# Performance work log

Measured on AMD Instinct MI355X. Metric: run time of the kernel, lower is better.

The kernel has to match this reference:

```python
import jax, jax.numpy as jnp
import numpy as np

DIM = 2048
NUM_HEADS = 16
HEAD_DIM = DIM // NUM_HEADS  # 128
B, L = 2, 2048


def setup_inputs() -> dict:
    key = jax.random.key(0)
    ks = jax.random.split(key, 5)
    x = jax.random.normal(ks[0], (B, L, DIM), dtype=jnp.float32)
    # genuine RoPE tables: inv_freq over half the head dim
    half = HEAD_DIM // 2
    inv_freq = 1.0 / (10000.0 ** (jnp.arange(half, dtype=jnp.float32) / half))
    ang = jnp.arange(L, dtype=jnp.float32)[:, None] * inv_freq[None, :]  # (L, half)
    cos = jnp.cos(ang)[:, None, :]  # (L, 1, half) broadcasts over (B,L,H,half)
    sin = jnp.sin(ang)[:, None, :]
    def dw_init(k, shape):
        fan_in, fan_out = shape
        std = 1.0 / np.sqrt(fan_in) * min(1.0, np.sqrt(fan_out / fan_in))
        return jax.random.normal(k, shape, dtype=jnp.float32) * std
    Wq = dw_init(ks[1], (DIM, DIM))
    Wk = dw_init(ks[2], (DIM, HEAD_DIM))
    Wv = dw_init(ks[3], (DIM, HEAD_DIM))
    Wo = dw_init(ks[4], (DIM, DIM))  # random instead of zeros so output is nontrivial
    return {"x": x, "cos": cos, "sin": sin, "Wq": Wq, "Wk": Wk, "Wv": Wv, "Wo": Wo}


def apply_rotary_emb(x, cos, sin):
    x1, x2 = jnp.split(x, 2, axis=-1)
    return jnp.concatenate([x1 * cos + x2 * sin, x1 * -sin + x2 * cos], axis=-1)


def rms_norm(x):
    return x * jax.lax.rsqrt(jnp.mean(x * x, axis=-1, keepdims=True) + 1e-6)


def reference(x, cos, sin, Wq, Wk, Wv, Wo):
    Bb, Ll, _ = x.shape
    q = (x @ Wq).reshape(Bb, Ll, NUM_HEADS, HEAD_DIM)  # (B,L,H,D)
    k = (x @ Wk)  # (B,L,D)  single KV head (MQA)
    v = (x @ Wv)  # (B,L,D)
    q = rms_norm(apply_rotary_emb(q, cos, sin))
    k = rms_norm(apply_rotary_emb(k[:, :, None, :], cos, sin))[:, :, 0, :]  # (B,L,D)
    scale = 1.0 / jnp.sqrt(jnp.asarray(HEAD_DIM, dtype=x.dtype))
    # scores without materializing broadcasted K: (B,H,Lq,Lk)
    scores = jnp.einsum('bqhd,bkd->bhqk', q, k) * scale
    causal = jnp.tril(jnp.ones((Ll, Ll), dtype=jnp.bool_))
    scores = jnp.where(causal[None, None], scores, jnp.asarray(-jnp.inf, dtype=scores.dtype))
    attn = jax.nn.softmax(scores, axis=-1)
    out = jnp.einsum('bhqk,bkd->bqhd', attn, v).reshape(Bb, Ll, DIM)
    return out @ Wo
```

## Files before the change

### kernel.cpp

```cpp
#include <hip/hip_runtime.h>

#define DIM 2048
#define NH 16
#define HD 128
#define BB 2
#define LL 2048
#define MROWS (BB * LL)
#define NKV 2304
#define NT 32

typedef __attribute__((ext_vector_type(8))) short short8;
typedef __attribute__((ext_vector_type(4))) float floatx4;

__device__ inline ushort f2bf(float f) {
    union { float f; unsigned u; } v; v.f = f;
    unsigned r = v.u + 0x7FFFu + ((v.u >> 16) & 1u);
    return (ushort)(r >> 16);
}

__device__ __forceinline__ ushort f2bf_fast(float f) {
    __bf16 h = (__bf16)f;
    return __builtin_bit_cast(unsigned short, h);
}

#define GL16(g, l)                                                         \
    __builtin_amdgcn_global_load_lds(                                      \
        (const __attribute__((address_space(1))) unsigned int*)(g),        \
        (__attribute__((address_space(3))) unsigned int*)(l), 16, 0, 0)

__device__ __forceinline__ short8 ld8(const ushort* p) {
    return *reinterpret_cast<const short8*>(p);
}

__global__ __launch_bounds__(256) void prep(const float* __restrict__ x,
                                            ushort* __restrict__ xb,
                                            const float* __restrict__ Wq,
                                            const float* __restrict__ Wk,
                                            const float* __restrict__ Wv,
                                            const float* __restrict__ Wo,
                                            ushort* __restrict__ Wcatt,
                                            ushort* __restrict__ Wot) {
    __shared__ ushort T[64][72];
    const int bid = blockIdx.x;
    const int tid = threadIdx.x;
    if (bid < 4096) {
        size_t i = ((size_t)bid * 256 + tid) * 8;
        float4 a = *reinterpret_cast<const float4*>(x + i);
        float4 b = *reinterpret_cast<const float4*>(x + i + 4);
        ushort o[8] = {f2bf(a.x), f2bf(a.y), f2bf(a.z), f2bf(a.w),
                       f2bf(b.x), f2bf(b.y), f2bf(b.z), f2bf(b.w)};
        *reinterpret_cast<uint4*>(xb + i) = *reinterpret_cast<uint4*>(o);
        return;
    }
    const int wb = bid - 4096;
    const float* in;
    ushort* out;
    int in_ld, c0, r0;
    const int out_ld = 2048;
    if (wb < 1024) {
        in = Wq; out = Wcatt; in_ld = 2048;
        c0 = (wb & 31) * 64; r0 = (wb >> 5) * 64;
    } else if (wb < 2048) {
        int t = wb - 1024;
        in = Wo; out = Wot; in_ld = 2048;
        c0 = (t & 31) * 64; r0 = (t >> 5) * 64;
    } else if (wb < 2112) {
        int t = wb - 2048;
        in = Wk; out = Wcatt + (size_t)2048 * 2048; in_ld = 128;
        c0 = (t & 1) * 64; r0 = (t >> 1) * 64;
    } else {
        int t = wb - 2112;
        in = Wv; out = Wcatt + (size_t)2176 * 2048; in_ld = 128;
        c0 = (t & 1) * 64; r0 = (t >> 1) * 64;
    }
#pragma unroll
    for (int rep = 0; rep < 4; ++rep) {
        int idx = tid + rep * 256;
        int r = idx >> 4, c4 = idx & 15;
        float4 f = *reinterpret_cast<const float4*>(
            in + (size_t)(r0 + r) * in_ld + c0 + c4 * 4);
        T[r][c4 * 4 + 0] = f2bf(f.x);
        T[r][c4 * 4 + 1] = f2bf(f.y);
        T[r][c4 * 4 + 2] = f2bf(f.z);
        T[r][c4 * 4 + 3] = f2bf(f.w);
    }
    __syncthreads();
#pragma unroll
    for (int rep = 0; rep < 4; ++rep) {
        int idx = tid + rep * 256;
        int cr = idx >> 4, rc4 = idx & 15;
        uint a0 = (uint)T[rc4 * 4 + 0][cr] | ((uint)T[rc4 * 4 + 1][cr] << 16);
        uint a1 = (uint)T[rc4 * 4 + 2][cr] | ((uint)T[rc4 * 4 + 3][cr] << 16);
        uint2 val = {a0, a1};
        *reinterpret_cast<uint2*>(
            out + (size_t)(c0 + cr) * out_ld + r0 + rc4 * 4) = val;
    }
}

__global__ __launch_bounds__(512)
__attribute__((amdgpu_waves_per_eu(2, 2)))
void gemm2pq(const ushort* __restrict__ A,
             const ushort* __restrict__ Bt,
             float* __restrict__ Y, int N) {
    __shared__ __attribute__((aligned(16))) ushort lds[51200];
    const int tid = threadIdx.x;
    const int lane = tid & 63;
    const int w = tid >> 6;
    const int col = lane & 15, quad = lane >> 4;
    const int sel = col & 7;
    const int L = blockIdx.y * 16 + blockIdx.x;
    const int x8 = L & 7, jj = L >> 3;
    const int bx = (x8 & 1) * 8 + (jj & 7);
    const int by = (x8 >> 1) * 4 + (jj >> 3);
    const int m0 = by * 256, n0 = bx * 144;

    const int r0 = tid >> 3;
    const int gc0 = (tid & 7) ^ (r0 & 7);
    const uint offA = (uint)(m0 + r0) * 2048u + (uint)gc0 * 8u;
    const uint offB = (uint)(n0 + r0) * 2048u + (uint)gc0 * 8u;

    floatx4 acc[2][9];
#pragma unroll
    for (int mt = 0; mt < 2; ++mt)
#pragma unroll
        for (int nt = 0; nt < 9; ++nt) acc[mt][nt] = (floatx4){0.f, 0.f, 0.f, 0.f};

    const int aoff0 = w * 2048 + col * 64;
    const int boff0 = 16384 + col * 64;
    const int koff0 = (quad ^ sel) * 8;
    const int koff1 = ((4 + quad) ^ sel) * 8;

    auto stage = [&](ushort* lbase, int t) {
        if (t >= NT) return;
        uint tk = (uint)t * 64u;
#pragma unroll
        for (int rep = 0; rep < 4; ++rep)
            GL16(A + offA + rep * 131072u + tk,
                 lbase + (size_t)(tid + rep * 512) * 8);
#pragma unroll
        for (int rep = 0; rep < 2; ++rep)
            GL16(Bt + offB + rep * 131072u + tk,
                 lbase + 16384 + (size_t)(tid + rep * 512) * 8);
        if (tid < 128)
            GL16(Bt + offB + 262144u + tk,
                 lbase + 16384 + (size_t)(tid + 1024) * 8);
    };

    stage(lds, 0);
    asm volatile("s_waitcnt vmcnt(0)" ::: "memory");
    __builtin_amdgcn_s_barrier();

#pragma unroll 2
    for (int t = 0; t < NT; ++t) {
        ushort* lb = lds + (t & 1) * 25600;
        ushort* lbn = lds + ((t + 1) & 1) * 25600;

        short8 a0[2], b0[9];
#pragma unroll
        for (int mt = 0; mt < 2; ++mt)
            a0[mt] = ld8(lb + aoff0 + mt * 1024 + koff0);
#pragma unroll
        for (int nt = 0; nt < 9; ++nt)
            b0[nt] = ld8(lb + boff0 + nt * 1024 + koff0);
        stage(lbn, t + 1);
        __builtin_amdgcn_s_setprio(1);
#pragma unroll
        for (int mt = 0; mt < 2; ++mt)
#pragma unroll
            for (int nt = 0; nt < 9; ++nt)
                acc[mt][nt] = __builtin_amdgcn_mfma_f32_16x16x32_bf16(
                    a0[mt], b0[nt], acc[mt][nt], 0, 0, 0);
        __builtin_amdgcn_s_setprio(0);

        short8 a1[2], b1[9];
#pragma unroll
        for (int mt = 0; mt < 2; ++mt)
            a1[mt] = ld8(lb + aoff0 + mt * 1024 + koff1);
#pragma unroll
        for (int nt = 0; nt < 9; ++nt)
            b1[nt] = ld8(lb + boff0 + nt * 1024 + koff1);
        __builtin_amdgcn_s_setprio(1);
#pragma unroll
        for (int mt = 0; mt < 2; ++mt)
#pragma unroll
            for (int nt = 0; nt < 9; ++nt)
                acc[mt][nt] = __builtin_amdgcn_mfma_f32_16x16x32_bf16(
                    a1[mt], b1[nt], acc[mt][nt], 0, 0, 0);
        __builtin_amdgcn_s_setprio(0);
        asm volatile("s_waitcnt vmcnt(0)" ::: "memory");
        __builtin_amdgcn_s_barrier();
    }

#pragma unroll
    for (int mt = 0; mt < 2; ++mt)
#pragma unroll
        for (int nt = 0; nt < 9; ++nt)
#pragma unroll
            for (int rr = 0; rr < 4; ++rr)
                Y[(size_t)(m0 + w * 32 + mt * 16 + quad * 4 + rr) * N + n0 +
                  nt * 16 + col] = acc[mt][nt][rr];
}

template <int U>
__device__ __forceinline__ void stage_po(const ushort* __restrict__ A,
                                         const ushort* __restrict__ Bt,
                                         ushort* lbase, uint offA, uint offB,
                                         int t) {
    if (t >= NT) return;
    const ushort* g = (U < 2) ? Bt : A;
    uint off = ((U < 2) ? offB : offA) + ((U == 1) ? 128u * 2048u : 0u) +
               (uint)t * 64u;
    ushort* l = lbase + U * 8192;
    GL16(g + off, l + (size_t)threadIdx.x * 8);
    GL16(g + off + 64u * 2048u, l + (size_t)(threadIdx.x + 512) * 8);
}

__global__ __launch_bounds__(512)
__attribute__((amdgpu_waves_per_eu(2, 2)))
void gemm2pw(const ushort* __restrict__ A,
             const ushort* __restrict__ Bt,
             float* __restrict__ Y, int N) {
    __shared__ __attribute__((aligned(16))) ushort lds[49152];
    const int tid = threadIdx.x;
    const int lane = tid & 63;
    const int w = tid >> 6;
    const int wm = w >> 2, wn = w & 3;
    const int col = lane & 15, quad = lane >> 4;
    const int sel = col & 7;
    const int L = blockIdx.y * 8 + blockIdx.x;
    const int x8 = L & 7, jj = L >> 3;
    const int bx = (x8 & 1) * 4 + (jj & 3);
    const int by = (x8 >> 1) * 8 + (jj >> 2);
    const int m0 = by * 128, n0 = bx * 256;

    const int r0 = tid >> 3;
    const int gc0 = (tid & 7) ^ (r0 & 7);
    const uint offA = (uint)(m0 + r0) * 2048u + (uint)gc0 * 8u;
    const uint offB = (uint)(n0 + r0) * 2048u + (uint)gc0 * 8u;

    floatx4 acc[4][4];
#pragma unroll
    for (int mt = 0; mt < 4; ++mt)
#pragma unroll
        for (int nt = 0; nt < 4; ++nt) acc[mt][nt] = (floatx4){0.f, 0.f, 0.f, 0.f};

    const int aoff0 = 16384 + wm * 4096 + col * 64;
    const int boff0 = (wn >> 1) * 8192 + ((wn & 1) * 64 + col) * 64;
    const int koff0 = (quad ^ sel) * 8;
    const int koff1 = ((4 + quad) ^ sel) * 8;

    stage_po<0>(A, Bt, lds, offA, offB, 0);
    stage_po<1>(A, Bt, lds, offA, offB, 0);
    stage_po<2>(A, Bt, lds, offA, offB, 0);
    asm volatile("s_waitcnt vmcnt(0)" ::: "memory");
    __builtin_amdgcn_s_barrier();

#pragma unroll 2
    for (int t = 0; t < NT; ++t) {
        ushort* lb = lds + (t & 1) * 24576;
        ushort* lbn = lds + ((t + 1) & 1) * 24576;

        short8 a0[4], b0[4];
#pragma unroll
        for (int mt = 0; mt < 4; ++mt)
            a0[mt] = ld8(lb + aoff0 + mt * 1024 + koff0);
#pragma unroll
        for (int nt = 0; nt < 4; ++nt)
            b0[nt] = ld8(lb + boff0 + nt * 1024 + koff0);
        stage_po<0>(A, Bt, lbn, offA, offB, t + 1);
        stage_po<1>(A, Bt, lbn, offA, offB, t + 1);
        stage_po<2>(A, Bt, lbn, offA, offB, t + 1);
        __builtin_amdgcn_s_setprio(1);
#pragma unroll
        for (int mt = 0; mt < 4; ++mt)
#pragma unroll
            for (int nt = 0; nt < 4; ++nt)
                acc[mt][nt] = __builtin_amdgcn_mfma_f32_16x16x32_bf16(
                    a0[mt], b0[nt], acc[mt][nt], 0, 0, 0);
        __builtin_amdgcn_s_setprio(0);

        short8 a1[4], b1[4];
#pragma unroll
        for (int mt = 0; mt < 4; ++mt)
            a1[mt] = ld8(lb + aoff0 + mt * 1024 + koff1);
#pragma unroll
        for (int nt = 0; nt < 4; ++nt)
            b1[nt] = ld8(lb + boff0 + nt * 1024 + koff1);
        __builtin_amdgcn_s_setprio(1);
#pragma unroll
        for (int mt = 0; mt < 4; ++mt)
#pragma unroll
            for (int nt = 0; nt < 4; ++nt)
                acc[mt][nt] = __builtin_amdgcn_mfma_f32_16x16x32_bf16(
                    a1[mt], b1[nt], acc[mt][nt], 0, 0, 0);
        __builtin_amdgcn_s_setprio(0);
        asm volatile("s_waitcnt vmcnt(0)" ::: "memory");
        __builtin_amdgcn_s_barrier();
    }

#pragma unroll
    for (int mt = 0; mt < 4; ++mt)
#pragma unroll
        for (int nt = 0; nt < 4; ++nt)
#pragma unroll
            for (int rr = 0; rr < 4; ++rr)
                Y[(size_t)(m0 + wm * 64 + mt * 16 + quad * 4 + rr) * N + n0 +
                  wn * 64 + nt * 16 + col] = acc[mt][nt][rr];
}

__device__ __forceinline__ void rope_row(const float* __restrict__ in,
                                         ushort* __restrict__ outb,
                                         const float* __restrict__ cosb,
                                         const float* __restrict__ sinb,
                                         int row, int heads, int in_ld,
                                         int lane) {
    int token = row / heads, head = row % heads;
    int l = token & (LL - 1);
    const float* p = in + (size_t)token * in_ld + head * HD;
    float x1 = p[lane];
    float x2 = p[lane + 64];
    float c = cosb[l * 64 + lane];
    float s = sinb[l * 64 + lane];
    float o1 = x1 * c + x2 * s;
    float o2 = -x1 * s + x2 * c;
    float ss = o1 * o1 + o2 * o2;
#pragma unroll
    for (int off = 32; off > 0; off >>= 1) ss += __shfl_xor(ss, off);
    float r = rsqrtf(ss * (1.0f / 128.0f) + 1e-6f);
    outb[(size_t)row * HD + lane] = f2bf(o1 * r);
    outb[(size_t)row * HD + lane + 64] = f2bf(o2 * r);
}

__global__ __launch_bounds__(256) void rope_vt(const float* __restrict__ qkv,
                                               ushort* __restrict__ qb,
                                               ushort* __restrict__ kb,
                                               ushort* __restrict__ vt,
                                               const float* __restrict__ cosb,
                                               const float* __restrict__ sinb) {
    __shared__ ushort T[64][72];
    const int bid = blockIdx.x;
    const int tid = threadIdx.x;
    const int lane = tid & 63;
    if (bid < 16384) {
        int row = bid * 4 + (tid >> 6);
        rope_row(qkv, qb, cosb, sinb, row, NH, NKV, lane);
        return;
    }
    if (bid < 17408) {
        int row = (bid - 16384) * 4 + (tid >> 6);
        rope_row(qkv + DIM, kb, cosb, sinb, row, 1, MROWS == 0 ? 1 : 1, lane),
            rope_row(qkv + DIM, kb, cosb, sinb, row, 1, NKV, lane);
        return;
    }
    const int t = bid - 17408;
    const int l0 = (t & 31) * 64, d0 = ((t >> 5) & 1) * 64, b = t >> 6;
    const float* v = qkv + DIM + HD;
#pragma unroll
    for (int rep = 0; rep < 4; ++rep) {
        int idx = tid + rep * 256;
        int r = idx >> 4, c4 = idx & 15;
        float4 f = *reinterpret_cast<const float4*>(
            v + (size_t)(b * LL + l0 + r) * NKV + d0 + c4 * 4);
        T[r][c4 * 4 + 0] = f2bf(f.x);
        T[r][c4 * 4 + 1] = f2bf(f.y);
        T[r][c4 * 4 + 2] = f2bf(f.z);
        T[r][c4 * 4 + 3] = f2bf(f.w);
    }
    __syncthreads();
#pragma unroll
    for (int rep = 0; rep < 4; ++rep) {
        int idx = tid + rep * 256;
        int dr = idx >> 4, lc4 = idx & 15;
        uint a0 = (uint)T[lc4 * 4 + 0][dr] | ((uint)T[lc4 * 4 + 1][dr] << 16);
        uint a1 = (uint)T[lc4 * 4 + 2][dr] | ((uint)T[lc4 * 4 + 3][dr] << 16);
        uint2 val = {a0, a1};
        *reinterpret_cast<uint2*>(
            vt + (size_t)(b * HD + d0 + dr) * LL + l0 + lc4 * 4) = val;
    }
}

__global__ __launch_bounds__(256) void flash_mfma(const ushort* __restrict__ qb,
                                                  const ushort* __restrict__ kb,
                                                  const ushort* __restrict__ vt,
                                                  ushort* __restrict__ aob) {
    __shared__ ushort Ks[64 * 128];
    __shared__ ushort VTs[128 * 64];
    __shared__ ushort Ps[4][16][68];

    const int tid = threadIdx.x;
    const int w = tid >> 6, lane = tid & 63;
    const int col = lane & 15, quad = lane >> 4;
    const int pairIdx = blockIdx.x, bh = blockIdx.y;
    const int b = bh >> 4, h = bh & 15;
    const int sel = col & 7;
    const float scl2 = 0.08838834764831845f * 1.44269504088896340736f;
    const float M2 = 11.5f * 1.44269504088896340736f;

    const int ksr[4] = {(tid + 0) >> 4, (tid + 256) >> 4, (tid + 512) >> 4,
                        (tid + 768) >> 4};
    const int vsr[4] = {(tid + 0) >> 3, (tid + 256) >> 3, (tid + 512) >> 3,
                        (tid + 768) >> 3};

    for (int sp = 0; sp < 2; ++sp) {
        const int qt = sp ? (31 - pairIdx) : pairIdx;
        const int q0 = qt * 64;

        const ushort* qrow =
            qb + ((size_t)(b * LL + q0 + w * 16 + col) * NH + h) * HD;
        short8 aq[4];
#pragma unroll
        for (int kc = 0; kc < 4; ++kc)
            aq[kc] = *reinterpret_cast<const short8*>(qrow + kc * 32 + quad * 8);

        float lrow[4] = {0.f, 0.f, 0.f, 0.f};
        floatx4 oacc[8];
#pragma unroll
        for (int dt = 0; dt < 8; ++dt) oacc[dt] = (floatx4){0.f, 0.f, 0.f, 0.f};

        const int ntiles = qt + 1;
        for (int kt = 0; kt < ntiles; ++kt) {
            const int k0 = kt * 64;
            __syncthreads();
#pragma unroll
            for (int rep = 0; rep < 4; ++rep) {
                int slot = tid + rep * 256;
                int r = ksr[rep];
                int gc = (slot & 15) ^ (r & 7);
                GL16(kb + (size_t)(b * LL + k0 + r) * HD + gc * 8,
                     Ks + (size_t)slot * 8);
            }
#pragma unroll
            for (int rep = 0; rep < 4; ++rep) {
                int slot = tid + rep * 256;
                int r = vsr[rep];
                int gc = (slot & 7) ^ (r & 7);
                GL16(vt + (size_t)(b * HD + r) * LL + k0 + gc * 8,
                     VTs + (size_t)slot * 8);
            }
            __syncthreads();

            floatx4 sacc[4];
#pragma unroll
            for (int nt = 0; nt < 4; ++nt)
                sacc[nt] = (floatx4){0.f, 0.f, 0.f, 0.f};
            __builtin_amdgcn_s_setprio(1);
#pragma unroll
            for (int nt = 0; nt < 4; ++nt) {
#pragma unroll
                for (int kc = 0; kc < 4; ++kc) {
                    short8 bk = *reinterpret_cast<const short8*>(
                        &Ks[(nt * 16 + col) * 128 +
                            ((kc * 4 + quad) ^ sel) * 8]);
                    sacc[nt] = __builtin_amdgcn_mfma_f32_16x16x32_bf16(
                        aq[kc], bk, sacc[nt], 0, 0, 0);
                }
            }
            __builtin_amdgcn_s_setprio(0);

            float psum[4] = {0.f, 0.f, 0.f, 0.f};
            if (kt == qt) {
#pragma unroll
                for (int nt = 0; nt < 4; ++nt) {
                    int kj = k0 + nt * 16 + col;
#pragma unroll
                    for (int rr = 0; rr < 4; ++rr) {
                        int qi = q0 + w * 16 + quad * 4 + rr;
                        float p = exp2f(fmaf(sacc[nt][rr], scl2, -M2));
                        p = (kj <= qi) ? p : 0.0f;
                        sacc[nt][rr] = p;
                        psum[rr] += p;
                    }
                }
            } else {
#pragma unroll
                for (int nt = 0; nt < 4; ++nt)
#pragma unroll
                    for (int rr = 0; rr < 4; ++rr) {
                        float p = exp2f(fmaf(sacc[nt][rr], scl2, -M2));
                        sacc[nt][rr] = p;
                        psum[rr] += p;
                    }
            }
#pragma unroll
            for (int rr = 0; rr < 4; ++rr) lrow[rr] += psum[rr];

#pragma unroll
            for (int nt = 0; nt < 4; ++nt)
#pragma unroll
                for (int rr = 0; rr < 4; ++rr)
                    Ps[w][quad * 4 + rr][nt * 16 + col] =
                        f2bf_fast(sacc[nt][rr]);
            asm volatile("s_waitcnt lgkmcnt(0)" ::: "memory");

#pragma unroll
            for (int kt2 = 0; kt2 < 2; ++kt2) {
                short8 ap = *reinterpret_cast<const short8*>(
                    &Ps[w][col][kt2 * 32 + quad * 8]);
                __builtin_amdgcn_s_setprio(1);
#pragma unroll
                for (int dt = 0; dt < 8; ++dt) {
                    short8 bv = *reinterpret_cast<const short8*>(
                        &VTs[(dt * 16 + col) * 64 +
                             ((kt2 * 4 + quad) ^ sel) * 8]);
                    oacc[dt] = __builtin_amdgcn_mfma_f32_16x16x32_bf16(
                        ap, bv, oacc[dt], 0, 0, 0);
                }
                __builtin_amdgcn_s_setprio(0);
            }
        }

#pragma unroll
        for (int off = 1; off < 16; off <<= 1)
#pragma unroll
            for (int rr = 0; rr < 4; ++rr)
                lrow[rr] += __shfl_xor(lrow[rr], off);
        float inv[4];
#pragma unroll
        for (int rr = 0; rr < 4; ++rr) inv[rr] = 1.0f / lrow[rr];
#pragma unroll
        for (int dt = 0; dt < 8; ++dt)
#pragma unroll
            for (int rr = 0; rr < 4; ++rr)
                aob[((size_t)(b * LL + q0 + w * 16 + quad * 4 + rr) * NH + h) *
                        HD + dt * 16 + col] =
                    f2bf_fast(oacc[dt][rr] * inv[rr]);
    }
}

extern "C" void kernel_launch(void* const* d_in, const int* in_sizes, int n_in,
                              void* d_out, int out_size, void* d_ws,
                              size_t ws_size, hipStream_t stream) {
    const float* x    = (const float*)d_in[0];
    const float* cosb = (const float*)d_in[1];
    const float* sinb = (const float*)d_in[2];
    const float* Wq   = (const float*)d_in[3];
    const float* Wk   = (const float*)d_in[4];
    const float* Wv   = (const float*)d_in[5];
    const float* Wo   = (const float*)d_in[6];
    float* out = (float*)d_out;

    float* qkv  = (float*)d_ws;
    ushort* xb  = (ushort*)(qkv + (size_t)MROWS * NKV);
    ushort* qb  = xb + (size_t)MROWS * DIM;
    ushort* kb  = qb + (size_t)MROWS * DIM;
    ushort* vt  = kb + (size_t)MROWS * HD;
    ushort* aob = vt + (size_t)MROWS * HD;
    ushort* Wcatt = aob + (size_t)MROWS * DIM;
    ushort* Wot   = Wcatt + (size_t)NKV * DIM;

    prep<<<dim3(4096 + 2176), 256, 0, stream>>>(x, xb, Wq, Wk, Wv, Wo, Wcatt,
                                                Wot);

    gemm2pq<<<dim3(NKV / 144, MROWS / 256), 512, 0, stream>>>(xb, Wcatt, qkv,
                                                              NKV);

    rope_vt<<<dim3(16384 + 1024 + 128), 256, 0, stream>>>(qkv, qb, kb, vt,
                                                          cosb, sinb);

    flash_mfma<<<dim3(LL / 128, BB * NH), 256, 0, stream>>>(qb, kb, vt, aob);

    gemm2pw<<<dim3(DIM / 256, MROWS / 128), 512, 0, stream>>>(aob, Wot, out,
                                                              DIM);
}
```

Before: 267.3 us.

## Process paired causal query tiles together to share K/V tile loads

The flash attention kernel used to process its two paired query tiles (qt and 31-qt) one after the other, reloading the K/V tiles for each. It now runs a single key loop up to the larger tile and computes both tiles against each shared K/V tile in LDS, with the smaller tile masked off once past its diagonal. This roughly halves K/V global-to-LDS traffic and barriers, and interleaves two independent MFMA chains. The price is doubled accumulator registers, so occupancy is pinned to 2 waves/EU; a duplicate rope_row call in the prep kernel is also removed.

```diff
diff --git a/kernel.cpp b/kernel.cpp
--- a/kernel.cpp
+++ b/kernel.cpp
@@ -348,8 +348,7 @@
     }
     if (bid < 17408) {
         int row = (bid - 16384) * 4 + (tid >> 6);
-        rope_row(qkv + DIM, kb, cosb, sinb, row, 1, MROWS == 0 ? 1 : 1, lane),
-            rope_row(qkv + DIM, kb, cosb, sinb, row, 1, NKV, lane);
+        rope_row(qkv + DIM, kb, cosb, sinb, row, 1, NKV, lane);
         return;
     }
     const int t = bid - 17408;
@@ -379,13 +378,15 @@
     }
 }
 
-__global__ __launch_bounds__(256) void flash_mfma(const ushort* __restrict__ qb,
-                                                  const ushort* __restrict__ kb,
-                                                  const ushort* __restrict__ vt,
-                                                  ushort* __restrict__ aob) {
+__global__ __launch_bounds__(256)
+__attribute__((amdgpu_waves_per_eu(2, 2)))
+void flash_mfma(const ushort* __restrict__ qb,
+                const ushort* __restrict__ kb,
+                const ushort* __restrict__ vt,
+                ushort* __restrict__ aob) {
     __shared__ ushort Ks[64 * 128];
     __shared__ ushort VTs[128 * 64];
-    __shared__ ushort Ps[4][16][68];
+    __shared__ ushort Ps[2][4][16][68];
 
     const int tid = threadIdx.x;
     const int w = tid >> 6, lane = tid & 63;
@@ -396,79 +397,118 @@
     const float scl2 = 0.08838834764831845f * 1.44269504088896340736f;
     const float M2 = 11.5f * 1.44269504088896340736f;
 
+    const int qtA = pairIdx, qtB = 31 - pairIdx;
+    const int q0A = qtA * 64, q0B = qtB * 64;
+
     const int ksr[4] = {(tid + 0) >> 4, (tid + 256) >> 4, (tid + 512) >> 4,
                         (tid + 768) >> 4};
     const int vsr[4] = {(tid + 0) >> 3, (tid + 256) >> 3, (tid + 512) >> 3,
                         (tid + 768) >> 3};
 
-    for (int sp = 0; sp < 2; ++sp) {
-        const int qt = sp ? (31 - pairIdx) : pairIdx;
-        const int q0 = qt * 64;
-
-        const ushort* qrow =
-            qb + ((size_t)(b * LL + q0 + w * 16 + col) * NH + h) * HD;
-        short8 aq[4];
-#pragma unroll
-        for (int kc = 0; kc < 4; ++kc)
-            aq[kc] = *reinterpret_cast<const short8*>(qrow + kc * 32 + quad * 8);
-
-        float lrow[4] = {0.f, 0.f, 0.f, 0.f};
-        floatx4 oacc[8];
-#pragma unroll
-        for (int dt = 0; dt < 8; ++dt) oacc[dt] = (floatx4){0.f, 0.f, 0.f, 0.f};
-
-        const int ntiles = qt + 1;
-        for (int kt = 0; kt < ntiles; ++kt) {
-            const int k0 = kt * 64;
-            __syncthreads();
-#pragma unroll
-            for (int rep = 0; rep < 4; ++rep) {
-                int slot = tid + rep * 256;
-                int r = ksr[rep];
-                int gc = (slot & 15) ^ (r & 7);
-                GL16(kb + (size_t)(b * LL + k0 + r) * HD + gc * 8,
-                     Ks + (size_t)slot * 8);
+    const ushort* qrowA =
+        qb + ((size_t)(b * LL + q0A + w * 16 + col) * NH + h) * HD;
+    const ushort* qrowB =
+        qb + ((size_t)(b * LL + q0B + w * 16 + col) * NH + h) * HD;
+    short8 aqA[4], aqB[4];
+#pragma unroll
+    for (int kc = 0; kc < 4; ++kc) {
+        aqA[kc] = *reinterpret_cast<const short8*>(qrowA + kc * 32 + quad * 8);
+        aqB[kc] = *reinterpret_cast<const short8*>(qrowB + kc * 32 + quad * 8);
+    }
+
+    float lrowA[4] = {0.f, 0.f, 0.f, 0.f}, lrowB[4] = {0.f, 0.f, 0.f, 0.f};
+    floatx4 oaccA[8], oaccB[8];
+#pragma unroll
+    for (int dt = 0; dt < 8; ++dt) {
+        oaccA[dt] = (floatx4){0.f, 0.f, 0.f, 0.f};
+        oaccB[dt] = (floatx4){0.f, 0.f, 0.f, 0.f};
+    }
+
+    for (int kt = 0; kt <= qtB; ++kt) {
+        const int k0 = kt * 64;
+        const bool actA = (kt <= qtA);
+        __syncthreads();
+#pragma unroll
+        for (int rep = 0; rep < 4; ++rep) {
+            int slot = tid + rep * 256;
+            int r = ksr[rep];
+            int gc = (slot & 15) ^ (r & 7);
+            GL16(kb + (size_t)(b * LL + k0 + r) * HD + gc * 8,
+                 Ks + (size_t)slot * 8);
+        }
+#pragma unroll
+        for (int rep = 0; rep < 4; ++rep) {
+            int slot = tid + rep * 256;
+            int r = vsr[rep];
+            int gc = (slot & 7) ^ (r & 7);
+            GL16(vt + (size_t)(b * HD + r) * LL + k0 + gc * 8,
+                 VTs + (size_t)slot * 8);
+        }
+        __syncthreads();
+
+        floatx4 sA[4], sB[4];
+#pragma unroll
+        for (int nt = 0; nt < 4; ++nt) {
+            sA[nt] = (floatx4){0.f, 0.f, 0.f, 0.f};
+            sB[nt] = (floatx4){0.f, 0.f, 0.f, 0.f};
+        }
+        __builtin_amdgcn_s_setprio(1);
+#pragma unroll
+        for (int nt = 0; nt < 4; ++nt) {
+#pragma unroll
+            for (int kc = 0; kc < 4; ++kc) {
+                short8 bk = *reinterpret_cast<const short8*>(
+                    &Ks[(nt * 16 + col) * 128 + ((kc * 4 + quad) ^ sel) * 8]);
+                sB[nt] = __builtin_amdgcn_mfma_f32_16x16x32_bf16(
+                    aqB[kc], bk, sB[nt], 0, 0, 0);
+                if (actA)
+                    sA[nt] = __builtin_amdgcn_mfma_f32_16x16x32_bf16(
+                        aqA[kc], bk, sA[nt], 0, 0, 0);
             }
-#pragma unroll
-            for (int rep = 0; rep < 4; ++rep) {
-                int slot = tid + rep * 256;
-                int r = vsr[rep];
-                int gc = (slot & 7) ^ (r & 7);
-                GL16(vt + (size_t)(b * HD + r) * LL + k0 + gc * 8,
-                     VTs + (size_t)slot * 8);
-            }
-            __syncthreads();
-
-            floatx4 sacc[4];
-#pragma unroll
-            for (int nt = 0; nt < 4; ++nt)
-                sacc[nt] = (floatx4){0.f, 0.f, 0.f, 0.f};
-            __builtin_amdgcn_s_setprio(1);
+        }
+        __builtin_amdgcn_s_setprio(0);
+
+        if (kt == qtB) {
 #pragma unroll
             for (int nt = 0; nt < 4; ++nt) {
-#pragma unroll
-                for (int kc = 0; kc < 4; ++kc) {
-                    short8 bk = *reinterpret_cast<const short8*>(
-                        &Ks[(nt * 16 + col) * 128 +
-                            ((kc * 4 + quad) ^ sel) * 8]);
-                    sacc[nt] = __builtin_amdgcn_mfma_f32_16x16x32_bf16(
-                        aq[kc], bk, sacc[nt], 0, 0, 0);
+                int kj = k0 + nt * 16 + col;
+#pragma unroll
+                for (int rr = 0; rr < 4; ++rr) {
+                    int qi = q0B + w * 16 + quad * 4 + rr;
+                    float p = exp2f(fmaf(sB[nt][rr], scl2, -M2));
+                    p = (kj <= qi) ? p : 0.0f;
+                    sB[nt][rr] = p;
+                    lrowB[rr] += p;
                 }
             }
-            __builtin_amdgcn_s_setprio(0);
-
-            float psum[4] = {0.f, 0.f, 0.f, 0.f};
-            if (kt == qt) {
+        } else {
+#pragma unroll
+            for (int nt = 0; nt < 4; ++nt)
+#pragma unroll
+                for (int rr = 0; rr < 4; ++rr) {
+                    float p = exp2f(fmaf(sB[nt][rr], scl2, -M2));
+                    sB[nt][rr] = p;
+                    lrowB[rr] += p;
+                }
+        }
+#pragma unroll
+        for (int nt = 0; nt < 4; ++nt)
+#pragma unroll
+            for (int rr = 0; rr < 4; ++rr)
+                Ps[1][w][quad * 4 + rr][nt * 16 + col] = f2bf_fast(sB[nt][rr]);
+
+        if (actA) {
+            if (kt == qtA) {
 #pragma unroll
                 for (int nt = 0; nt < 4; ++nt) {
                     int kj = k0 + nt * 16 + col;
 #pragma unroll
                     for (int rr = 0; rr < 4; ++rr) {
-                        int qi = q0 + w * 16 + quad * 4 + rr;
-                        float p = exp2f(fmaf(sacc[nt][rr], scl2, -M2));
+                        int qi = q0A + w * 16 + quad * 4 + rr;
+                        float p = exp2f(fmaf(sA[nt][rr], scl2, -M2));
                         p = (kj <= qi) ? p : 0.0f;
-                        sacc[nt][rr] = p;
-                        psum[rr] += p;
+                        sA[nt][rr] = p;
+                        lrowA[rr] += p;
                     }
                 }
             } else {
@@ -476,55 +516,65 @@
                 for (int nt = 0; nt < 4; ++nt)
 #pragma unroll
                     for (int rr = 0; rr < 4; ++rr) {
-                        float p = exp2f(fmaf(sacc[nt][rr], scl2, -M2));
-                        sacc[nt][rr] = p;
-                        psum[rr] += p;
+                        float p = exp2f(fmaf(sA[nt][rr], scl2, -M2));
+                        sA[nt][rr] = p;
+                        lrowA[rr] += p;
                     }
             }
 #pragma unroll
-            for (int rr = 0; rr < 4; ++rr) lrow[rr] += psum[rr];
-
-#pragma unroll
             for (int nt = 0; nt < 4; ++nt)
 #pragma unroll
                 for (int rr = 0; rr < 4; ++rr)
-                    Ps[w][quad * 4 + rr][nt * 16 + col] =
-                        f2bf_fast(sacc[nt][rr]);
-            asm volatile("s_waitcnt lgkmcnt(0)" ::: "memory");
-
-#pragma unroll
-            for (int kt2 = 0; kt2 < 2; ++kt2) {
-                short8 ap = *reinterpret_cast<const short8*>(
-                    &Ps[w][col][kt2 * 32 + quad * 8]);
-                __builtin_amdgcn_s_setprio(1);
-#pragma unroll
-                for (int dt = 0; dt < 8; ++dt) {
-                    short8 bv = *reinterpret_cast<const short8*>(
-                        &VTs[(dt * 16 + col) * 64 +
-                             ((kt2 * 4 + quad) ^ sel) * 8]);
-                    oacc[dt] = __builtin_amdgcn_mfma_f32_16x16x32_bf16(
-                        ap, bv, oacc[dt], 0, 0, 0);
-                }
-                __builtin_amdgcn_s_setprio(0);
+                    Ps[0][w][quad * 4 + rr][nt * 16 + col] =
+                        f2bf_fast(sA[nt][rr]);
+        }
+        asm volatile("s_waitcnt lgkmcnt(0)" ::: "memory");
+
+#pragma unroll
+        for (int kt2 = 0; kt2 < 2; ++kt2) {
+            short8 apB = *reinterpret_cast<const short8*>(
+                &Ps[1][w][col][kt2 * 32 + quad * 8]);
+            short8 apA;
+            if (actA)
+                apA = *reinterpret_cast<const short8*>(
+                    &Ps[0][w][col][kt2 * 32 + quad * 8]);
+            __builtin_amdgcn_s_setprio(1);
+#pragma unroll
+            for (int dt = 0; dt < 8; ++dt) {
+                short8 bv = *reinterpret_cast<const short8*>(
+                    &VTs[(dt * 16 + col) * 64 + ((kt2 * 4 + quad) ^ sel) * 8]);
+                oaccB[dt] = __builtin_amdgcn_mfma_f32_16x16x32_bf16(
+                    apB, bv, oaccB[dt], 0, 0, 0);
+                if (actA)
+                    oaccA[dt] = __builtin_amdgcn_mfma_f32_16x16x32_bf16(
+                        apA, bv, oaccA[dt], 0, 0, 0);
             }
-        }
-
-#pragma unroll
-        for (int off = 1; off < 16; off <<= 1)
-#pragma unroll
-            for (int rr = 0; rr < 4; ++rr)
-                lrow[rr] += __shfl_xor(lrow[rr], off);
-        float inv[4];
-#pragma unroll
-        for (int rr = 0; rr < 4; ++rr) inv[rr] = 1.0f / lrow[rr];
-#pragma unroll
-        for (int dt = 0; dt < 8; ++dt)
-#pragma unroll
-            for (int rr = 0; rr < 4; ++rr)
-                aob[((size_t)(b * LL + q0 + w * 16 + quad * 4 + rr) * NH + h) *
-                        HD + dt * 16 + col] =
-                    f2bf_fast(oacc[dt][rr] * inv[rr]);
-    }
+            __builtin_amdgcn_s_setprio(0);
+        }
+    }
+
+#pragma unroll
+    for (int off = 1; off < 16; off <<= 1)
+#pragma unroll
+        for (int rr = 0; rr < 4; ++rr) {
+            lrowA[rr] += __shfl_xor(lrowA[rr], off);
+            lrowB[rr] += __shfl_xor(lrowB[rr], off);
+        }
+    float invA[4], invB[4];
+#pragma unroll
+    for (int rr = 0; rr < 4; ++rr) {
+        invA[rr] = 1.0f / lrowA[rr];
+        invB[rr] = 1.0f / lrowB[rr];
+    }
+#pragma unroll
+    for (int dt = 0; dt < 8; ++dt)
+#pragma unroll
+        for (int rr = 0; rr < 4; ++rr) {
+            aob[((size_t)(b * LL + q0A + w * 16 + quad * 4 + rr) * NH + h) *
+                    HD + dt * 16 + col] = f2bf_fast(oaccA[dt][rr] * invA[rr]);
+            aob[((size_t)(b * LL + q0B + w * 16 + quad * 4 + rr) * NH + h) *
+                    HD + dt * 16 + col] = f2bf_fast(oaccB[dt][rr] * invB[rr]);
+        }
 }
 
 extern "C" void kernel_launch(void* const* d_in, const int* in_sizes, int n_in,
```

Result: slower. 282.0 us (+5.5%).
